# Kernel tuning notes

Hardware: AMD Instinct MI355X
Metric: run time of the kernel (lower is better)

The kernel has to match this reference:

```python
import jax, jax.numpy as jnp
import numpy as np

N = 50000        # node_num
E = 1600000      # num edges (avg degree 32)
IN_DIM = 128
OUT_DIM = 64
SLOPE = 0.1      # leaky relu slope_ratio
EPS = 1e-12


def setup_inputs() -> dict:
    key = jax.random.key(0)
    k0, k1, k2, k3 = jax.random.split(key, 4)
    x = jax.random.normal(k0, (N, IN_DIM), dtype=jnp.float32)
    edge_index = jax.random.randint(k1, (2, E), 0, N, dtype=jnp.int64)
    # Linear(in_dim, out_dim) params
    W = jax.random.normal(k2, (OUT_DIM, IN_DIM), dtype=jnp.float32) * (1.0 / np.sqrt(IN_DIM))
    b = jnp.zeros((OUT_DIM,), dtype=jnp.float32)
    # attention vector a: [2*out_dim, 1], kaiming-normal-ish init
    a = jax.random.normal(k3, (2 * OUT_DIM, 1), dtype=jnp.float32) * np.sqrt(2.0 / (2 * OUT_DIM))
    return {"x": x, "edge_index": edge_index, "W": W, "b": b, "a": a}


def reference(x, edge_index, W, b, a):
    # new_embeddings = Linear(x)
    new = x @ W.T + b                          # [N, OUT_DIM]
    src = edge_index[0]
    dst = edge_index[1]
    # cat(new[src], new[dst]) @ a  ==  new[src]@a_src + new[dst]@a_dst (avoids [E, 2*OUT] intermediate)
    a_src = a[:OUT_DIM, 0]                     # [OUT_DIM]
    a_dst = a[OUT_DIM:, 0]                     # [OUT_DIM]
    score = new[src] @ a_src + new[dst] @ a_dst  # [E]
    e = jnp.exp(jax.nn.leaky_relu(score, SLOPE))  # [E]
    # spmm(A, ones) -> per-row sum of edge weights; spmm(A, new) -> weighted aggregation
    row_sum = jax.ops.segment_sum(e, src, num_segments=N)                 # [N]
    results = jax.ops.segment_sum(e[:, None] * new[dst], src, num_segments=N)  # [N, OUT_DIM]
    return results / (row_sum[:, None] + EPS)
```

## Files before the change

### kernel.cpp

```cpp
#include <hip/hip_runtime.h>
#include <hip/hip_bf16.h>

#define NN    50000
#define EE    1600000
#define IND   128
#define OUTD  64
#define SLOPE 0.1f

#define BSH    5
#define BW     32
#define NB     1564
#define NFINE  1568
#define CAP    1408
#define CAPT   6
#define CSH    8
#define NC     196
#define CAP1   8832
#define NBLK1  500
#define CHUNK1 (EE / NBLK1)
#define NSPLIT 4
#define SCAP   (CAP1 / NSPLIT)

typedef __attribute__((ext_vector_type(8))) short short8;
typedef __attribute__((ext_vector_type(4))) float float4v;

__global__ __launch_bounds__(256) void linear_kernel(
    const float* __restrict__ x, const float* __restrict__ W,
    const float* __restrict__ bias, const float* __restrict__ a,
    ushort* __restrict__ nbuf2, float* __restrict__ s_src, float* __restrict__ s_dst)
{
    __shared__ ushort xs[16 * 136];
    __shared__ ushort wt[64 * 136];
    __shared__ float  newt[16 * 68];
    const int tid = threadIdx.x;
    const int node0 = blockIdx.x * 16;

    const float4* W4 = (const float4*)W;
    #pragma unroll
    for (int i = 0; i < 8; ++i) {
        int idx = tid + i * 256;
        float4 wv = W4[idx];
        int n = idx >> 5, k = (idx & 31) * 4;
        ushort4 pk; __hip_bfloat16 h;
        h = __float2bfloat16(wv.x); pk.x = *(ushort*)&h;
        h = __float2bfloat16(wv.y); pk.y = *(ushort*)&h;
        h = __float2bfloat16(wv.z); pk.z = *(ushort*)&h;
        h = __float2bfloat16(wv.w); pk.w = *(ushort*)&h;
        *(ushort4*)&wt[n * 136 + k] = pk;
    }
    const float4* x4 = (const float4*)(x + (size_t)node0 * IND);
    #pragma unroll
    for (int i = 0; i < 2; ++i) {
        int idx = tid + i * 256;
        float4 xv = x4[idx];
        int r = idx >> 5, cc = (idx & 31) * 4;
        ushort4 pk; __hip_bfloat16 h;
        h = __float2bfloat16(xv.x); pk.x = *(ushort*)&h;
        h = __float2bfloat16(xv.y); pk.y = *(ushort*)&h;
        h = __float2bfloat16(xv.z); pk.z = *(ushort*)&h;
        h = __float2bfloat16(xv.w); pk.w = *(ushort*)&h;
        *(ushort4*)&xs[r * 136 + cc] = pk;
    }
    __syncthreads();

    const int w    = tid >> 6;
    const int lane = tid & 63;
    const int q    = lane >> 4;
    const int m16  = lane & 15;
    float4v acc = {0.f, 0.f, 0.f, 0.f};
    #pragma unroll
    for (int kk = 0; kk < IND; kk += 32) {
        short8 af = *(const short8*)&xs[m16 * 136 + kk + q * 8];
        short8 bf = *(const short8*)&wt[(w * 16 + m16) * 136 + kk + q * 8];
        acc = __builtin_amdgcn_mfma_f32_16x16x32_bf16(af, bf, acc, 0, 0, 0);
    }
    const float bv = bias[w * 16 + m16];
    #pragma unroll
    for (int r = 0; r < 4; ++r)
        newt[(q * 4 + r) * 68 + w * 16 + m16] = acc[r] + bv;
    __syncthreads();

    const int nl = tid >> 4;
    const int jg = tid & 15;
    const int j0 = jg * 4;
    float4 va = *(const float4*)&newt[nl * 68 + j0];
    const int n = node0 + nl;
    ushort4 pk;
    { __hip_bfloat16 h;
      h = __float2bfloat16(va.x); pk.x = *(ushort*)&h;
      h = __float2bfloat16(va.y); pk.y = *(ushort*)&h;
      h = __float2bfloat16(va.z); pk.z = *(ushort*)&h;
      h = __float2bfloat16(va.w); pk.w = *(ushort*)&h; }
    *(ushort4*)&nbuf2[(size_t)n * OUTD + j0] = pk;

    float ss = va.x * a[j0]        + va.y * a[j0 + 1]
             + va.z * a[j0 + 2]    + va.w * a[j0 + 3];
    float sd = va.x * a[OUTD + j0]     + va.y * a[OUTD + j0 + 1]
             + va.z * a[OUTD + j0 + 2] + va.w * a[OUTD + j0 + 3];
    #pragma unroll
    for (int m = 1; m < 16; m <<= 1) {
        ss += __shfl_xor(ss, m, 64);
        sd += __shfl_xor(sd, m, 64);
    }
    if (jg == 0) { s_src[n] = ss; s_dst[n] = sd; }
}

__global__ __launch_bounds__(256) void coarsebin_kernel(const int* __restrict__ ei,
                                                        int* __restrict__ gcur1,
                                                        unsigned* __restrict__ ebuf1)
{
    __shared__ int h[NC];
    for (int i = threadIdx.x; i < NC; i += 256) h[i] = 0;
    __syncthreads();
    const int base = blockIdx.x * CHUNK1;
    const int4* s4p = (const int4*)(ei + base);
    for (int i = threadIdx.x; i < CHUNK1 / 4; i += 256) {
        int4 s4 = s4p[i];
        atomicAdd(&h[s4.x >> CSH], 1);
        atomicAdd(&h[s4.y >> CSH], 1);
        atomicAdd(&h[s4.z >> CSH], 1);
        atomicAdd(&h[s4.w >> CSH], 1);
    }
    __syncthreads();
    for (int i = threadIdx.x; i < NC; i += 256) {
        int c = h[i];
        if (c) h[i] = i * CAP1 + atomicAdd(&gcur1[i * 16], c);
    }
    __syncthreads();
    const int4* d4p = (const int4*)(ei + EE + base);
    for (int i = threadIdx.x; i < CHUNK1 / 4; i += 256) {
        int4 s4 = s4p[i];
        int4 d4 = d4p[i];
        int p0 = atomicAdd(&h[s4.x >> CSH], 1);
        int p1 = atomicAdd(&h[s4.y >> CSH], 1);
        int p2 = atomicAdd(&h[s4.z >> CSH], 1);
        int p3 = atomicAdd(&h[s4.w >> CSH], 1);
        ebuf1[p0] = ((unsigned)(s4.x & 255) << 16) | (unsigned)d4.x;
        ebuf1[p1] = ((unsigned)(s4.y & 255) << 16) | (unsigned)d4.y;
        ebuf1[p2] = ((unsigned)(s4.z & 255) << 16) | (unsigned)d4.z;
        ebuf1[p3] = ((unsigned)(s4.w & 255) << 16) | (unsigned)d4.w;
    }
}

__global__ __launch_bounds__(256) void finebin_kernel(
    const unsigned* __restrict__ ebuf1, const int* __restrict__ gcur1,
    int* __restrict__ gcur2, unsigned* __restrict__ ebuf2)
{
    __shared__ unsigned stage[SCAP];
    __shared__ int h[8], lofs[8], grun[8], cur[8];
    const int tid = threadIdx.x;
    const int c   = blockIdx.x >> 2;
    const int sp  = blockIdx.x & 3;
    const int cnt1 = gcur1[c * 16];
    const int seg  = (cnt1 + NSPLIT - 1) / NSPLIT;
    const int lo   = sp * seg;
    const int m    = max(0, min(cnt1, lo + seg) - lo);
    if (tid < 8) h[tid] = 0;
    __syncthreads();
    const unsigned* eb = ebuf1 + (size_t)c * CAP1 + lo;
    for (int i = tid; i < m; i += 256)
        atomicAdd(&h[eb[i] >> 21], 1);
    __syncthreads();
    if (tid == 0) {
        int run = 0;
        #pragma unroll
        for (int f = 0; f < 8; ++f) { lofs[f] = run; run += h[f]; }
    }
    __syncthreads();
    if (tid < 8) {
        cur[tid]  = lofs[tid];
        grun[tid] = atomicAdd(&gcur2[(c * 8 + tid) * 16], h[tid]);
    }
    __syncthreads();
    for (int i = tid; i < m; i += 256) {
        unsigned e = eb[i];
        int pos = atomicAdd(&cur[e >> 21], 1);
        stage[pos] = (((e >> 16) & 31u) << 16) | (e & 0xFFFFu);
    }
    __syncthreads();
    #pragma unroll 1
    for (int f = 0; f < 8; ++f) {
        const int cf = h[f];
        unsigned* dst = ebuf2 + (size_t)(c * 8 + f) * CAP + grun[f];
        const unsigned* sp2 = stage + lofs[f];
        for (int i = tid; i < cf; i += 256) dst[i] = sp2[i];
    }
}

__global__ __launch_bounds__(256) void aggregate_kernel(
    const unsigned* __restrict__ ebuf, const int* __restrict__ gcur,
    const ushort* __restrict__ nbuf2,
    const float* __restrict__ s_src, const float* __restrict__ s_dst,
    float* __restrict__ out)
{
    __shared__ uint2 pairs[CAP];
    __shared__ float ssL[BW];
    __shared__ int cntL[BW], ofs[BW], cur[BW];
    const int tid  = threadIdx.x;
    const int wid  = tid >> 6;
    const int lane = tid & 63;
    const int b    = blockIdx.x;
    const int n0   = b << BSH;
    const unsigned* __restrict__ nbuf4 = (const unsigned*)nbuf2;

    if (tid < BW) {
        int n = n0 + tid;
        ssL[tid]  = (n < NN) ? s_src[n] : 0.f;
        cntL[tid] = 0;
    }
    __syncthreads();

    const int cnt = gcur[b * 16];
    const unsigned* eb = ebuf + (size_t)b * CAP;

    unsigned er[CAPT]; float evr[CAPT];
    int nk = 0;
    for (int i = tid; i < cnt; i += 256) {
        unsigned e = eb[i];
        int d  = e & 0xFFFFu;
        int ln = e >> 16;
        float sc = ssL[ln] + s_dst[d];
        float lr = sc > 0.f ? sc : SLOPE * sc;
        er[nk] = e; evr[nk] = __expf(lr); ++nk;
        atomicAdd(&cntL[ln], 1);
    }
    __syncthreads();

    if (wid == 0) {
        int c = (lane < BW) ? cntL[lane] : 0;
        int sc = c;
        #pragma unroll
        for (int m = 1; m < BW; m <<= 1) {
            int v = __shfl_up(sc, m, 64);
            if (lane >= m) sc += v;
        }
        if (lane < BW) { ofs[lane] = sc - c; cur[lane] = sc - c; }
    }
    __syncthreads();

    for (int k = 0; k < nk; ++k) {
        int ln = er[k] >> 16;
        int pos = atomicAdd(&cur[ln], 1);
        pairs[pos] = make_uint2(er[k] & 0xFFFFu, __float_as_uint(evr[k]));
    }
    __syncthreads();

    const int h32 = lane >> 5;
    const int c32 = lane & 31;

    #pragma unroll 1
    for (int t = 0; t < BW / 4; ++t) {
        const int ln  = wid * (BW / 4) + t;
        const int beg = ofs[ln];
        const int len = cntL[ln];

        float accL = 0.f, accH = 0.f, es = 0.f;
        int j = 0;
        for (; j + 8 <= len; j += 8) {
            uint2 pA = pairs[beg + j + 0 + h32];
            uint2 pB = pairs[beg + j + 2 + h32];
            uint2 pC = pairs[beg + j + 4 + h32];
            uint2 pD = pairs[beg + j + 6 + h32];
            unsigned gA = nbuf4[pA.x * 32 + c32];
            unsigned gB = nbuf4[pB.x * 32 + c32];
            unsigned gC = nbuf4[pC.x * 32 + c32];
            unsigned gD = nbuf4[pD.x * 32 + c32];
            float fA = __uint_as_float(pA.y), fB = __uint_as_float(pB.y);
            float fC = __uint_as_float(pC.y), fD = __uint_as_float(pD.y);
            es += fA + fB + fC + fD;
            accL = fmaf(fA, __uint_as_float(gA << 16), accL);
            accH = fmaf(fA, __uint_as_float(gA & 0xFFFF0000u), accH);
            accL = fmaf(fB, __uint_as_float(gB << 16), accL);
            accH = fmaf(fB, __uint_as_float(gB & 0xFFFF0000u), accH);
            accL = fmaf(fC, __uint_as_float(gC << 16), accL);
            accH = fmaf(fC, __uint_as_float(gC & 0xFFFF0000u), accH);
            accL = fmaf(fD, __uint_as_float(gD << 16), accL);
            accH = fmaf(fD, __uint_as_float(gD & 0xFFFF0000u), accH);
        }
        for (; j < len; j += 2) {
            int idx = j + h32;
            uint2 p = pairs[beg + min(idx, len - 1)];
            float f = (idx < len) ? __uint_as_float(p.y) : 0.f;
            unsigned g = nbuf4[p.x * 32 + c32];
            es += f;
            accL = fmaf(f, __uint_as_float(g << 16), accL);
            accH = fmaf(f, __uint_as_float(g & 0xFFFF0000u), accH);
        }
        es   += __shfl_xor(es, 32, 64);
        accL += __shfl_xor(accL, 32, 64);
        accH += __shfl_xor(accH, 32, 64);
        const int n = n0 + ln;
        if (h32 == 0 && n < NN) {
            float inv = 1.f / (es + 1e-12f);
            float2 o = make_float2(accL * inv, accH * inv);
            *(float2*)&out[(size_t)n * OUTD + 2 * c32] = o;
        }
    }
}

extern "C" void kernel_launch(void* const* d_in, const int* in_sizes, int n_in,
                              void* d_out, int out_size, void* d_ws, size_t ws_size,
                              hipStream_t stream) {
    const float* x  = (const float*)d_in[0];
    const int*   ei = (const int*)d_in[1];
    const float* W  = (const float*)d_in[2];
    const float* b  = (const float*)d_in[3];
    const float* a  = (const float*)d_in[4];
    float* out = (float*)d_out;

    ushort*   nbuf2 = (ushort*)d_ws;
    float*    s_src = (float*)(nbuf2 + (size_t)NN * OUTD);
    float*    s_dst = s_src + NN;
    int*      gcur1 = (int*)(s_dst + NN);
    int*      gcur2 = gcur1 + NC * 16;
    unsigned* ebuf1 = (unsigned*)(gcur2 + NFINE * 16);
    unsigned* ebuf2 = ebuf1 + (size_t)NC * CAP1;

    hipMemsetAsync(gcur1, 0, (NC + NFINE) * 16 * sizeof(int), stream);
    linear_kernel<<<NN / 16, 256, 0, stream>>>(x, W, b, a, nbuf2, s_src, s_dst);
    coarsebin_kernel<<<NBLK1, 256, 0, stream>>>(ei, gcur1, ebuf1);
    finebin_kernel<<<NC * NSPLIT, 256, 0, stream>>>(ebuf1, gcur1, gcur2, ebuf2);
    aggregate_kernel<<<NB, 256, 0, stream>>>(ebuf2, gcur2, nbuf2, s_src, s_dst, out);
}
```

Baseline: 150.5 us.

## Fuse linear and coarse-bin kernels; widen aggregate gathers to 8-byte loads

Merges the linear projection and the coarse edge-binning kernels into one launch. The first NBLK1 blocks do binning and the rest do the linear layer, with shared memory shared through a union. This removes one launch and lets the two independent stages run at the same time. Separately, the aggregate kernel now has each lane load 4 bf16 features as a uint2 and processes 4 edges per wave in parallel instead of 2, which needs a two-step cross-lane reduction and gives wider gathers and output stores.

```diff
diff --git a/kernel.cpp b/kernel.cpp
--- a/kernel.cpp
+++ b/kernel.cpp
@@ -20,21 +20,66 @@
 #define CHUNK1 (EE / NBLK1)
 #define NSPLIT 4
 #define SCAP   (CAP1 / NSPLIT)
+#define NLIN   (NN / 16)
 
 typedef __attribute__((ext_vector_type(8))) short short8;
 typedef __attribute__((ext_vector_type(4))) float float4v;
 
-__global__ __launch_bounds__(256) void linear_kernel(
+union SMem {
+    struct {
+        ushort xs[16 * 136];
+        ushort wt[64 * 136];
+        float  newt[16 * 68];
+    } lin;
+    int h[NC];
+};
+
+__global__ __launch_bounds__(256) void fused_lincoarse_kernel(
     const float* __restrict__ x, const float* __restrict__ W,
     const float* __restrict__ bias, const float* __restrict__ a,
+    const int* __restrict__ ei, int* __restrict__ gcur1,
+    unsigned* __restrict__ ebuf1,
     ushort* __restrict__ nbuf2, float* __restrict__ s_src, float* __restrict__ s_dst)
 {
-    __shared__ ushort xs[16 * 136];
-    __shared__ ushort wt[64 * 136];
-    __shared__ float  newt[16 * 68];
+    __shared__ SMem sm;
     const int tid = threadIdx.x;
-    const int node0 = blockIdx.x * 16;
-
+
+    if (blockIdx.x < NBLK1) {
+        int* h = sm.h;
+        for (int i = tid; i < NC; i += 256) h[i] = 0;
+        __syncthreads();
+        const int base = blockIdx.x * CHUNK1;
+        const int4* s4p = (const int4*)(ei + base);
+        for (int i = tid; i < CHUNK1 / 4; i += 256) {
+            int4 s4 = s4p[i];
+            atomicAdd(&h[s4.x >> CSH], 1);
+            atomicAdd(&h[s4.y >> CSH], 1);
+            atomicAdd(&h[s4.z >> CSH], 1);
+            atomicAdd(&h[s4.w >> CSH], 1);
+        }
+        __syncthreads();
+        for (int i = tid; i < NC; i += 256) {
+            int c = h[i];
+            if (c) h[i] = i * CAP1 + atomicAdd(&gcur1[i * 16], c);
+        }
+        __syncthreads();
+        const int4* d4p = (const int4*)(ei + EE + base);
+        for (int i = tid; i < CHUNK1 / 4; i += 256) {
+            int4 s4 = s4p[i];
+            int4 d4 = d4p[i];
+            int p0 = atomicAdd(&h[s4.x >> CSH], 1);
+            int p1 = atomicAdd(&h[s4.y >> CSH], 1);
+            int p2 = atomicAdd(&h[s4.z >> CSH], 1);
+            int p3 = atomicAdd(&h[s4.w >> CSH], 1);
+            ebuf1[p0] = ((unsigned)(s4.x & 255) << 16) | (unsigned)d4.x;
+            ebuf1[p1] = ((unsigned)(s4.y & 255) << 16) | (unsigned)d4.y;
+            ebuf1[p2] = ((unsigned)(s4.z & 255) << 16) | (unsigned)d4.z;
+            ebuf1[p3] = ((unsigned)(s4.w & 255) << 16) | (unsigned)d4.w;
+        }
+        return;
+    }
+
+    const int node0 = (blockIdx.x - NBLK1) * 16;
     const float4* W4 = (const float4*)W;
     #pragma unroll
     for (int i = 0; i < 8; ++i) {
@@ -46,7 +91,7 @@
         h = __float2bfloat16(wv.y); pk.y = *(ushort*)&h;
         h = __float2bfloat16(wv.z); pk.z = *(ushort*)&h;
         h = __float2bfloat16(wv.w); pk.w = *(ushort*)&h;
-        *(ushort4*)&wt[n * 136 + k] = pk;
+        *(ushort4*)&sm.lin.wt[n * 136 + k] = pk;
     }
     const float4* x4 = (const float4*)(x + (size_t)node0 * IND);
     #pragma unroll
@@ -59,7 +104,7 @@
         h = __float2bfloat16(xv.y); pk.y = *(ushort*)&h;
         h = __float2bfloat16(xv.z); pk.z = *(ushort*)&h;
         h = __float2bfloat16(xv.w); pk.w = *(ushort*)&h;
-        *(ushort4*)&xs[r * 136 + cc] = pk;
+        *(ushort4*)&sm.lin.xs[r * 136 + cc] = pk;
     }
     __syncthreads();
 
@@ -70,20 +115,20 @@
     float4v acc = {0.f, 0.f, 0.f, 0.f};
     #pragma unroll
     for (int kk = 0; kk < IND; kk += 32) {
-        short8 af = *(const short8*)&xs[m16 * 136 + kk + q * 8];
-        short8 bf = *(const short8*)&wt[(w * 16 + m16) * 136 + kk + q * 8];
+        short8 af = *(const short8*)&sm.lin.xs[m16 * 136 + kk + q * 8];
+        short8 bf = *(const short8*)&sm.lin.wt[(w * 16 + m16) * 136 + kk + q * 8];
         acc = __builtin_amdgcn_mfma_f32_16x16x32_bf16(af, bf, acc, 0, 0, 0);
     }
     const float bv = bias[w * 16 + m16];
     #pragma unroll
     for (int r = 0; r < 4; ++r)
-        newt[(q * 4 + r) * 68 + w * 16 + m16] = acc[r] + bv;
+        sm.lin.newt[(q * 4 + r) * 68 + w * 16 + m16] = acc[r] + bv;
     __syncthreads();
 
     const int nl = tid >> 4;
     const int jg = tid & 15;
     const int j0 = jg * 4;
-    float4 va = *(const float4*)&newt[nl * 68 + j0];
+    float4 va = *(const float4*)&sm.lin.newt[nl * 68 + j0];
     const int n = node0 + nl;
     ushort4 pk;
     { __hip_bfloat16 h;
@@ -103,43 +148,6 @@
         sd += __shfl_xor(sd, m, 64);
     }
     if (jg == 0) { s_src[n] = ss; s_dst[n] = sd; }
-}
-
-__global__ __launch_bounds__(256) void coarsebin_kernel(const int* __restrict__ ei,
-                                                        int* __restrict__ gcur1,
-                                                        unsigned* __restrict__ ebuf1)
-{
-    __shared__ int h[NC];
-    for (int i = threadIdx.x; i < NC; i += 256) h[i] = 0;
-    __syncthreads();
-    const int base = blockIdx.x * CHUNK1;
-    const int4* s4p = (const int4*)(ei + base);
-    for (int i = threadIdx.x; i < CHUNK1 / 4; i += 256) {
-        int4 s4 = s4p[i];
-        atomicAdd(&h[s4.x >> CSH], 1);
-        atomicAdd(&h[s4.y >> CSH], 1);
-        atomicAdd(&h[s4.z >> CSH], 1);
-        atomicAdd(&h[s4.w >> CSH], 1);
-    }
-    __syncthreads();
-    for (int i = threadIdx.x; i < NC; i += 256) {
-        int c = h[i];
-        if (c) h[i] = i * CAP1 + atomicAdd(&gcur1[i * 16], c);
-    }
-    __syncthreads();
-    const int4* d4p = (const int4*)(ei + EE + base);
-    for (int i = threadIdx.x; i < CHUNK1 / 4; i += 256) {
-        int4 s4 = s4p[i];
-        int4 d4 = d4p[i];
-        int p0 = atomicAdd(&h[s4.x >> CSH], 1);
-        int p1 = atomicAdd(&h[s4.y >> CSH], 1);
-        int p2 = atomicAdd(&h[s4.z >> CSH], 1);
-        int p3 = atomicAdd(&h[s4.w >> CSH], 1);
-        ebuf1[p0] = ((unsigned)(s4.x & 255) << 16) | (unsigned)d4.x;
-        ebuf1[p1] = ((unsigned)(s4.y & 255) << 16) | (unsigned)d4.y;
-        ebuf1[p2] = ((unsigned)(s4.z & 255) << 16) | (unsigned)d4.z;
-        ebuf1[p3] = ((unsigned)(s4.w & 255) << 16) | (unsigned)d4.w;
-    }
 }
 
 __global__ __launch_bounds__(256) void finebin_kernel(
@@ -201,7 +209,7 @@
     const int lane = tid & 63;
     const int b    = blockIdx.x;
     const int n0   = b << BSH;
-    const unsigned* __restrict__ nbuf4 = (const unsigned*)nbuf2;
+    const uint2* __restrict__ nbufq = (const uint2*)nbuf2;
 
     if (tid < BW) {
         int n = n0 + tid;
@@ -245,8 +253,8 @@
     }
     __syncthreads();
 
-    const int h32 = lane >> 5;
-    const int c32 = lane & 31;
+    const int e16 = lane >> 4;
+    const int c16 = lane & 15;
 
     #pragma unroll 1
     for (int t = 0; t < BW / 4; ++t) {
@@ -254,46 +262,58 @@
         const int beg = ofs[ln];
         const int len = cntL[ln];
 
-        float accL = 0.f, accH = 0.f, es = 0.f;
+        float a0 = 0.f, a1 = 0.f, a2 = 0.f, a3 = 0.f, es = 0.f;
         int j = 0;
-        for (; j + 8 <= len; j += 8) {
-            uint2 pA = pairs[beg + j + 0 + h32];
-            uint2 pB = pairs[beg + j + 2 + h32];
-            uint2 pC = pairs[beg + j + 4 + h32];
-            uint2 pD = pairs[beg + j + 6 + h32];
-            unsigned gA = nbuf4[pA.x * 32 + c32];
-            unsigned gB = nbuf4[pB.x * 32 + c32];
-            unsigned gC = nbuf4[pC.x * 32 + c32];
-            unsigned gD = nbuf4[pD.x * 32 + c32];
+        for (; j + 16 <= len; j += 16) {
+            uint2 pA = pairs[beg + j + 0  + e16];
+            uint2 pB = pairs[beg + j + 4  + e16];
+            uint2 pC = pairs[beg + j + 8  + e16];
+            uint2 pD = pairs[beg + j + 12 + e16];
+            uint2 gA = nbufq[pA.x * 16 + c16];
+            uint2 gB = nbufq[pB.x * 16 + c16];
+            uint2 gC = nbufq[pC.x * 16 + c16];
+            uint2 gD = nbufq[pD.x * 16 + c16];
             float fA = __uint_as_float(pA.y), fB = __uint_as_float(pB.y);
             float fC = __uint_as_float(pC.y), fD = __uint_as_float(pD.y);
             es += fA + fB + fC + fD;
-            accL = fmaf(fA, __uint_as_float(gA << 16), accL);
-            accH = fmaf(fA, __uint_as_float(gA & 0xFFFF0000u), accH);
-            accL = fmaf(fB, __uint_as_float(gB << 16), accL);
-            accH = fmaf(fB, __uint_as_float(gB & 0xFFFF0000u), accH);
-            accL = fmaf(fC, __uint_as_float(gC << 16), accL);
-            accH = fmaf(fC, __uint_as_float(gC & 0xFFFF0000u), accH);
-            accL = fmaf(fD, __uint_as_float(gD << 16), accL);
-            accH = fmaf(fD, __uint_as_float(gD & 0xFFFF0000u), accH);
-        }
-        for (; j < len; j += 2) {
-            int idx = j + h32;
+            a0 = fmaf(fA, __uint_as_float(gA.x << 16), a0);
+            a1 = fmaf(fA, __uint_as_float(gA.x & 0xFFFF0000u), a1);
+            a2 = fmaf(fA, __uint_as_float(gA.y << 16), a2);
+            a3 = fmaf(fA, __uint_as_float(gA.y & 0xFFFF0000u), a3);
+            a0 = fmaf(fB, __uint_as_float(gB.x << 16), a0);
+            a1 = fmaf(fB, __uint_as_float(gB.x & 0xFFFF0000u), a1);
+            a2 = fmaf(fB, __uint_as_float(gB.y << 16), a2);
+            a3 = fmaf(fB, __uint_as_float(gB.y & 0xFFFF0000u), a3);
+            a0 = fmaf(fC, __uint_as_float(gC.x << 16), a0);
+            a1 = fmaf(fC, __uint_as_float(gC.x & 0xFFFF0000u), a1);
+            a2 = fmaf(fC, __uint_as_float(gC.y << 16), a2);
+            a3 = fmaf(fC, __uint_as_float(gC.y & 0xFFFF0000u), a3);
+            a0 = fmaf(fD, __uint_as_float(gD.x << 16), a0);
+            a1 = fmaf(fD, __uint_as_float(gD.x & 0xFFFF0000u), a1);
+            a2 = fmaf(fD, __uint_as_float(gD.y << 16), a2);
+            a3 = fmaf(fD, __uint_as_float(gD.y & 0xFFFF0000u), a3);
+        }
+        for (; j < len; j += 4) {
+            int idx = j + e16;
             uint2 p = pairs[beg + min(idx, len - 1)];
             float f = (idx < len) ? __uint_as_float(p.y) : 0.f;
-            unsigned g = nbuf4[p.x * 32 + c32];
+            uint2 g = nbufq[p.x * 16 + c16];
             es += f;
-            accL = fmaf(f, __uint_as_float(g << 16), accL);
-            accH = fmaf(f, __uint_as_float(g & 0xFFFF0000u), accH);
-        }
-        es   += __shfl_xor(es, 32, 64);
-        accL += __shfl_xor(accL, 32, 64);
-        accH += __shfl_xor(accH, 32, 64);
+            a0 = fmaf(f, __uint_as_float(g.x << 16), a0);
+            a1 = fmaf(f, __uint_as_float(g.x & 0xFFFF0000u), a1);
+            a2 = fmaf(f, __uint_as_float(g.y << 16), a2);
+            a3 = fmaf(f, __uint_as_float(g.y & 0xFFFF0000u), a3);
+        }
+        es += __shfl_xor(es, 16, 64); es += __shfl_xor(es, 32, 64);
+        a0 += __shfl_xor(a0, 16, 64); a0 += __shfl_xor(a0, 32, 64);
+        a1 += __shfl_xor(a1, 16, 64); a1 += __shfl_xor(a1, 32, 64);
+        a2 += __shfl_xor(a2, 16, 64); a2 += __shfl_xor(a2, 32, 64);
+        a3 += __shfl_xor(a3, 16, 64); a3 += __shfl_xor(a3, 32, 64);
         const int n = n0 + ln;
-        if (h32 == 0 && n < NN) {
+        if (e16 == 0 && n < NN) {
             float inv = 1.f / (es + 1e-12f);
-            float2 o = make_float2(accL * inv, accH * inv);
-            *(float2*)&out[(size_t)n * OUTD + 2 * c32] = o;
+            float4 o = make_float4(a0 * inv, a1 * inv, a2 * inv, a3 * inv);
+            *(float4*)&out[(size_t)n * OUTD + c16 * 4] = o;
         }
     }
 }
@@ -317,8 +337,8 @@
     unsigned* ebuf2 = ebuf1 + (size_t)NC * CAP1;
 
     hipMemsetAsync(gcur1, 0, (NC + NFINE) * 16 * sizeof(int), stream);
-    linear_kernel<<<NN / 16, 256, 0, stream>>>(x, W, b, a, nbuf2, s_src, s_dst);
-    coarsebin_kernel<<<NBLK1, 256, 0, stream>>>(ei, gcur1, ebuf1);
+    fused_lincoarse_kernel<<<NBLK1 + NLIN, 256, 0, stream>>>(
+        x, W, b, a, ei, gcur1, ebuf1, nbuf2, s_src, s_dst);
     finebin_kernel<<<NC * NSPLIT, 256, 0, stream>>>(ebuf1, gcur1, gcur2, ebuf2);
     aggregate_kernel<<<NB, 256, 0, stream>>>(ebuf2, gcur2, nbuf2, s_src, s_dst, out);
 }
```

Measured after the change: 146.6 us. 1.03x faster.
